# Kernel tuning notes

Hardware: AMD Instinct MI355X
Metric: run time of the kernel (lower is better)

## Reference

```python
import jax, jax.numpy as jnp
import numpy as np

LN2 = 0.6931471805599453
PI = 3.14159265

def ssp(x):
    # shifted softplus: log(exp(x)+1) - log(2)
    return jax.nn.softplus(x) - LN2

def setup_inputs() -> dict:
    key = jax.random.key(0)
    ks = jax.random.split(key, 16)
    N, E, R, F = 50000, 800000, 300, 64
    edge_index = jax.random.randint(ks[0], (2, E), 0, N, dtype=jnp.int64)
    node_feature = jax.random.normal(ks[1], (N, F), dtype=jnp.float32)
    rbf_tensor = jax.random.uniform(ks[2], (E, R), dtype=jnp.float32)
    cutoff = jnp.float32(10.0)
    dist = jax.random.uniform(ks[3], (E, 1), dtype=jnp.float32) * cutoff
    s = lambda fan_in: 1.0 / np.sqrt(fan_in)
    fw1 = jax.random.uniform(ks[4], (R, F), jnp.float32, -s(R), s(R))
    fb1 = jax.random.uniform(ks[5], (F,), jnp.float32, -s(R), s(R))
    fw2 = jax.random.uniform(ks[6], (F, F), jnp.float32, -s(F), s(F))
    fb2 = jax.random.uniform(ks[7], (F,), jnp.float32, -s(F), s(F))
    l1w = jax.random.uniform(ks[8], (F, F), jnp.float32, -s(F), s(F))
    l1b = jax.random.uniform(ks[9], (F,), jnp.float32, -s(F), s(F))
    l2w = jax.random.uniform(ks[10], (F, F), jnp.float32, -s(F), s(F))
    l2b = jax.random.uniform(ks[11], (F,), jnp.float32, -s(F), s(F))
    l3w = jax.random.uniform(ks[12], (F, F), jnp.float32, -s(F), s(F))
    l3b = jax.random.uniform(ks[13], (F,), jnp.float32, -s(F), s(F))
    return {"edge_index": edge_index, "node_feature": node_feature,
            "rbf_tensor": rbf_tensor, "dist": dist, "cutoff": cutoff,
            "fw1": fw1, "fb1": fb1, "fw2": fw2, "fb2": fb2,
            "l1w": l1w, "l1b": l1b, "l2w": l2w, "l2b": l2b,
            "l3w": l3w, "l3b": l3b}

def reference(edge_index, node_feature, rbf_tensor, dist, cutoff,
              fw1, fb1, fw2, fb2, l1w, l1b, l2w, l2b, l3w, l3b):
    N = node_feature.shape[0]
    x0 = node_feature  # residual
    h = node_feature @ l1w + l1b  # linear1: [N, F]
    # filter generator: two linear + shifted softplus layers on edge RBFs
    w = ssp(rbf_tensor @ fw1 + fb1)  # [E, F]
    w = ssp(w @ fw2 + fb2)           # [E, F]
    # cosine cutoff modulation ([E,1] broadcasts over F)
    w = w * (1.0 + jnp.cos(PI * dist / cutoff))
    # cfconv with flow='target_to_source': gather x_j from edge_index[1],
    # scatter-add into edge_index[0]
    msg = h[edge_index[1]] * w  # [E, F]
    agg = jax.ops.segment_sum(msg, edge_index[0], num_segments=N)  # [N, F]
    out = agg @ l2w + l2b
    out = ssp(out)
    out = out @ l3w + l3b
    return out + x0
```

## Files before the change

### kernel.cpp

```cpp
#include <hip/hip_runtime.h>
#include <hip/hip_bf16.h>
#include <math.h>

#define NNODES 50000
#define NEDGES 800000
#define RDIM   300
#define KPAD   320
#define LDA    328
#define LDW    72

typedef __attribute__((ext_vector_type(8))) short short8;
typedef __attribute__((ext_vector_type(4))) float floatx4;

__device__ __forceinline__ float ssp(float x) {
    return fmaxf(x, 0.0f) + log1pf(expf(-fabsf(x))) - 0.69314718056f;
}

__device__ __forceinline__ unsigned short f2bf(float f) {
    unsigned int u = __float_as_uint(f);
    unsigned int r = (u + 0x7FFFu + ((u >> 16) & 1u)) >> 16;
    return (unsigned short)r;
}

__global__ void prep_weights(const float* __restrict__ fw1, const float* __restrict__ fw2,
                             unsigned short* __restrict__ fw1t, unsigned short* __restrict__ fw2t) {
    int t = threadIdx.x + blockIdx.x * blockDim.x;
    int stride = blockDim.x * gridDim.x;
    for (int idx = t; idx < 64 * KPAD; idx += stride) {
        int n = idx / KPAD, k = idx - n * KPAD;
        float v = (k < RDIM) ? fw1[k * 64 + n] : 0.0f;
        fw1t[idx] = f2bf(v);
    }
    for (int idx = t; idx < 64 * 64; idx += stride) {
        int n = idx >> 6, k = idx & 63;
        fw2t[idx] = f2bf(fw2[k * 64 + n]);
    }
}

__global__ __launch_bounds__(256) void linear1_kernel(const float* __restrict__ x,
    const float* __restrict__ w, const float* __restrict__ b, float* __restrict__ h) {
    __shared__ float xs[64][65];
    __shared__ float ws[64][65];
    int t = threadIdx.x;
    int r0 = blockIdx.x * 64;
    for (int i = t; i < 4096; i += 256) ws[i >> 6][i & 63] = w[i];
    for (int i = t; i < 4096; i += 256) {
        int r = i >> 6;
        xs[r][i & 63] = (r0 + r < NNODES) ? x[(size_t)(r0 + r) * 64 + (i & 63)] : 0.0f;
    }
    __syncthreads();
    int c = t & 63;
    int rb = t >> 6;
    float bias = b[c];
    #pragma unroll 4
    for (int ri = 0; ri < 16; ri++) {
        int r = rb * 16 + ri;
        float acc = bias;
        #pragma unroll
        for (int k = 0; k < 64; k++) acc += xs[r][k] * ws[k][c];
        if (r0 + r < NNODES) h[(size_t)(r0 + r) * 64 + c] = acc;
    }
}

__global__ __launch_bounds__(256) void edge_kernel(
    const int* __restrict__ ei,
    const float* __restrict__ rbf,
    const float* __restrict__ dist,
    const float* __restrict__ cutoffp,
    const unsigned short* __restrict__ fw1t,
    const float* __restrict__ fb1,
    const unsigned short* __restrict__ fw2t,
    const float* __restrict__ fb2,
    const float* __restrict__ h,
    float* __restrict__ agg)
{
    __shared__ __align__(16) unsigned short rbf_s[64 * LDA];
    __shared__ __align__(16) unsigned short w1_s[64 * LDW];
    __shared__ float cut_s[64];
    __shared__ int src_s[64], dst_s[64];

    const int t = threadIdx.x;
    const int e0 = blockIdx.x * 64;
    const int lane = t & 63;
    const int wv = t >> 6;

    if (t < 64) {
        int e = e0 + t;
        dst_s[t] = ei[e];
        src_s[t] = ei[NEDGES + e];
        float co = *cutoffp;
        cut_s[t] = 1.0f + cosf(3.14159265f * dist[e] / co);
    }

    const int n = (wv << 4) + (lane & 15);
    const int kb = (lane >> 4) << 3;
    short8 b1[10];
    #pragma unroll
    for (int ks = 0; ks < 10; ks++)
        b1[ks] = *(const short8*)&fw1t[n * KPAD + ks * 32 + kb];
    short8 b2[2];
    #pragma unroll
    for (int ks = 0; ks < 2; ks++)
        b2[ks] = *(const short8*)&fw2t[n * 64 + ks * 32 + kb];
    const float fb1n = fb1[n];
    const float fb2n = fb2[n];

    {
        const float4* rp = (const float4*)(rbf + (size_t)e0 * RDIM);
        #pragma unroll
        for (int i = 0; i < 19; i++) {
            int idx4 = t + 256 * i;
            if (idx4 < 4800) {
                float4 v = rp[idx4];
                int row = idx4 / 75;
                int col4 = idx4 - row * 75;
                unsigned long long packed =
                    (unsigned long long)f2bf(v.x)
                  | ((unsigned long long)f2bf(v.y) << 16)
                  | ((unsigned long long)f2bf(v.z) << 32)
                  | ((unsigned long long)f2bf(v.w) << 48);
                *(unsigned long long*)&rbf_s[row * LDA + col4 * 4] = packed;
            }
        }
        if (t < 64) {
            #pragma unroll
            for (int c4 = 75; c4 < 80; c4++)
                *(unsigned long long*)&rbf_s[t * LDA + c4 * 4] = 0ULL;
        }
    }
    __syncthreads();

    const floatx4 zero4 = {0.0f, 0.0f, 0.0f, 0.0f};
    floatx4 acc[4] = {zero4, zero4, zero4, zero4};
    const int arow = lane & 15;
    #pragma unroll
    for (int ks = 0; ks < 10; ks++) {
        #pragma unroll
        for (int mt = 0; mt < 4; mt++) {
            short8 a = *(const short8*)&rbf_s[(mt * 16 + arow) * LDA + ks * 32 + kb];
            acc[mt] = __builtin_amdgcn_mfma_f32_16x16x32_bf16(a, b1[ks], acc[mt], 0, 0, 0);
        }
    }

    #pragma unroll
    for (int mt = 0; mt < 4; mt++) {
        #pragma unroll
        for (int r = 0; r < 4; r++) {
            int edge = mt * 16 + ((lane >> 4) << 2) + r;
            float v = ssp(acc[mt][r] + fb1n);
            w1_s[edge * LDW + n] = f2bf(v);
        }
    }
    __syncthreads();

    floatx4 acc2[4] = {zero4, zero4, zero4, zero4};
    #pragma unroll
    for (int ks = 0; ks < 2; ks++) {
        #pragma unroll
        for (int mt = 0; mt < 4; mt++) {
            short8 a = *(const short8*)&w1_s[(mt * 16 + arow) * LDW + ks * 32 + kb];
            acc2[mt] = __builtin_amdgcn_mfma_f32_16x16x32_bf16(a, b2[ks], acc2[mt], 0, 0, 0);
        }
    }

    #pragma unroll
    for (int mt = 0; mt < 4; mt++) {
        #pragma unroll
        for (int r = 0; r < 4; r++) {
            int el = mt * 16 + ((lane >> 4) << 2) + r;
            float w2v = ssp(acc2[mt][r] + fb2n) * cut_s[el];
            float msg = w2v * h[(size_t)src_s[el] * 64 + n];
            atomicAdd(&agg[(size_t)dst_s[el] * 64 + n], msg);
        }
    }
}

__global__ __launch_bounds__(256) void output_kernel(float* __restrict__ out,
    const float* __restrict__ x0,
    const float* __restrict__ l2w, const float* __restrict__ l2b,
    const float* __restrict__ l3w, const float* __restrict__ l3b) {
    __shared__ float as[64][65];
    __shared__ float w2s[64][65];
    __shared__ float w3s[64][65];
    __shared__ float ts[64][65];
    int t = threadIdx.x;
    int r0 = blockIdx.x * 64;
    for (int i = t; i < 4096; i += 256) w2s[i >> 6][i & 63] = l2w[i];
    for (int i = t; i < 4096; i += 256) w3s[i >> 6][i & 63] = l3w[i];
    for (int i = t; i < 4096; i += 256) {
        int r = i >> 6;
        as[r][i & 63] = (r0 + r < NNODES) ? out[(size_t)(r0 + r) * 64 + (i & 63)] : 0.0f;
    }
    __syncthreads();
    int c = t & 63;
    int rb = t >> 6;
    float b2 = l2b[c];
    #pragma unroll 4
    for (int ri = 0; ri < 16; ri++) {
        int r = rb * 16 + ri;
        float acc = b2;
        #pragma unroll
        for (int k = 0; k < 64; k++) acc += as[r][k] * w2s[k][c];
        ts[r][c] = ssp(acc);
    }
    __syncthreads();
    float b3 = l3b[c];
    #pragma unroll 4
    for (int ri = 0; ri < 16; ri++) {
        int r = rb * 16 + ri;
        float acc = b3;
        #pragma unroll
        for (int k = 0; k < 64; k++) acc += ts[r][k] * w3s[k][c];
        if (r0 + r < NNODES)
            out[(size_t)(r0 + r) * 64 + c] = acc + x0[(size_t)(r0 + r) * 64 + c];
    }
}

extern "C" void kernel_launch(void* const* d_in, const int* in_sizes, int n_in,
                              void* d_out, int out_size, void* d_ws, size_t ws_size,
                              hipStream_t stream) {
    const int* ei              = (const int*)d_in[0];
    const float* node_feature  = (const float*)d_in[1];
    const float* rbf           = (const float*)d_in[2];
    const float* dist          = (const float*)d_in[3];
    const float* cutoff        = (const float*)d_in[4];
    const float* fw1           = (const float*)d_in[5];
    const float* fb1           = (const float*)d_in[6];
    const float* fw2           = (const float*)d_in[7];
    const float* fb2           = (const float*)d_in[8];
    const float* l1w           = (const float*)d_in[9];
    const float* l1b           = (const float*)d_in[10];
    const float* l2w           = (const float*)d_in[11];
    const float* l2b           = (const float*)d_in[12];
    const float* l3w           = (const float*)d_in[13];
    const float* l3b           = (const float*)d_in[14];

    unsigned short* fw1t = (unsigned short*)d_ws;
    unsigned short* fw2t = (unsigned short*)((char*)d_ws + 40960);
    float* h = (float*)((char*)d_ws + 49152);
    float* agg = (float*)d_out;

    hipMemsetAsync(d_out, 0, (size_t)out_size * sizeof(float), stream);
    prep_weights<<<64, 256, 0, stream>>>(fw1, fw2, fw1t, fw2t);
    linear1_kernel<<<(NNODES + 63) / 64, 256, 0, stream>>>(node_feature, l1w, l1b, h);
    edge_kernel<<<NEDGES / 64, 256, 0, stream>>>(ei, rbf, dist, cutoff, fw1t, fb1, fw2t, fb2, h, agg);
    output_kernel<<<(NNODES + 63) / 64, 256, 0, stream>>>(agg, node_feature, l2w, l2b, l3w, l3b);
}
```

Baseline: 1.599 ms.

## Sort edges by destination and pre-reduce messages before atomic scatter

Builds a destination-sorted edge permutation via histogram, single-block scan and atomic scatter, then processes edges in sorted order. Messages are staged in shared memory and each wave reduces runs of equal destinations before issuing one atomic per run. This targets the cost of per-element global atomics, at the price of extra preprocessing kernels, a serial one-block scan, and gathered rather than contiguous rbf row reads.

```diff
diff --git a/kernel.cpp b/kernel.cpp
--- a/kernel.cpp
+++ b/kernel.cpp
@@ -8,6 +8,7 @@
 #define KPAD   320
 #define LDA    328
 #define LDW    72
+#define MSG_LD 66
 
 typedef __attribute__((ext_vector_type(8))) short short8;
 typedef __attribute__((ext_vector_type(4))) float floatx4;
@@ -62,8 +63,51 @@
     }
 }
 
+__global__ __launch_bounds__(256) void hist_kernel(const int* __restrict__ ei,
+                                                   int* __restrict__ deg) {
+    int e = threadIdx.x + blockIdx.x * 256;
+    if (e < NEDGES) atomicAdd(&deg[ei[e]], 1);
+}
+
+__global__ __launch_bounds__(1024) void scan_kernel(const int* __restrict__ deg,
+                                                    int* __restrict__ cursor) {
+    __shared__ int buf[1024];
+    __shared__ int base_s;
+    int t = threadIdx.x;
+    if (t == 0) base_s = 0;
+    __syncthreads();
+    for (int tile = 0; tile < NNODES; tile += 1024) {
+        int idx = tile + t;
+        int v = (idx < NNODES) ? deg[idx] : 0;
+        buf[t] = v;
+        __syncthreads();
+        for (int off = 1; off < 1024; off <<= 1) {
+            int self = buf[t];
+            int x = (t >= off) ? buf[t - off] : 0;
+            __syncthreads();
+            buf[t] = self + x;
+            __syncthreads();
+        }
+        if (idx < NNODES) cursor[idx] = base_s + buf[t] - v;
+        __syncthreads();
+        if (t == 0) base_s += buf[1023];
+        __syncthreads();
+    }
+}
+
+__global__ __launch_bounds__(256) void scatter_kernel(const int* __restrict__ ei,
+                                                      int* __restrict__ cursor,
+                                                      int* __restrict__ perm) {
+    int e = threadIdx.x + blockIdx.x * 256;
+    if (e < NEDGES) {
+        int slot = atomicAdd(&cursor[ei[e]], 1);
+        perm[slot] = e;
+    }
+}
+
 __global__ __launch_bounds__(256) void edge_kernel(
     const int* __restrict__ ei,
+    const int* __restrict__ perm,
     const float* __restrict__ rbf,
     const float* __restrict__ dist,
     const float* __restrict__ cutoffp,
@@ -77,7 +121,9 @@
     __shared__ __align__(16) unsigned short rbf_s[64 * LDA];
     __shared__ __align__(16) unsigned short w1_s[64 * LDW];
     __shared__ float cut_s[64];
-    __shared__ int src_s[64], dst_s[64];
+    __shared__ int src_s[64], dst_s[64], ep_s[64];
+
+    float (*msg_s)[MSG_LD] = (float (*)[MSG_LD])rbf_s;
 
     const int t = threadIdx.x;
     const int e0 = blockIdx.x * 64;
@@ -85,7 +131,8 @@
     const int wv = t >> 6;
 
     if (t < 64) {
-        int e = e0 + t;
+        int e = perm[e0 + t];
+        ep_s[t] = e;
         dst_s[t] = ei[e];
         src_s[t] = ei[NEDGES + e];
         float co = *cutoffp;
@@ -105,15 +152,17 @@
     const float fb1n = fb1[n];
     const float fb2n = fb2[n];
 
+    __syncthreads();
+
     {
-        const float4* rp = (const float4*)(rbf + (size_t)e0 * RDIM);
         #pragma unroll
         for (int i = 0; i < 19; i++) {
             int idx4 = t + 256 * i;
             if (idx4 < 4800) {
-                float4 v = rp[idx4];
                 int row = idx4 / 75;
                 int col4 = idx4 - row * 75;
+                const float4* rowp = (const float4*)(rbf + (size_t)ep_s[row] * RDIM);
+                float4 v = rowp[col4];
                 unsigned long long packed =
                     (unsigned long long)f2bf(v.x)
                   | ((unsigned long long)f2bf(v.y) << 16)
@@ -169,9 +218,27 @@
         for (int r = 0; r < 4; r++) {
             int el = mt * 16 + ((lane >> 4) << 2) + r;
             float w2v = ssp(acc2[mt][r] + fb2n) * cut_s[el];
-            float msg = w2v * h[(size_t)src_s[el] * 64 + n];
-            atomicAdd(&agg[(size_t)dst_s[el] * 64 + n], msg);
-        }
+            msg_s[el][n] = w2v * h[(size_t)src_s[el] * 64 + n];
+        }
+    }
+    __syncthreads();
+
+    {
+        const int c = lane;
+        const int r0 = wv * 16;
+        int cur = dst_s[r0];
+        float acc3 = 0.0f;
+        #pragma unroll
+        for (int r = r0; r < r0 + 16; ++r) {
+            int d = dst_s[r];
+            if (d != cur) {
+                atomicAdd(&agg[(size_t)cur * 64 + c], acc3);
+                acc3 = 0.0f;
+                cur = d;
+            }
+            acc3 += msg_s[r][c];
+        }
+        atomicAdd(&agg[(size_t)cur * 64 + c], acc3);
     }
 }
 
@@ -237,12 +304,20 @@
 
     unsigned short* fw1t = (unsigned short*)d_ws;
     unsigned short* fw2t = (unsigned short*)((char*)d_ws + 40960);
-    float* h = (float*)((char*)d_ws + 49152);
+    float* h    = (float*)((char*)d_ws + 49152);
+    int*   deg  = (int*)((char*)d_ws + 12849152);
+    int*   curs = (int*)((char*)d_ws + 13049152);
+    int*   perm = (int*)((char*)d_ws + 13249152);
     float* agg = (float*)d_out;
 
     hipMemsetAsync(d_out, 0, (size_t)out_size * sizeof(float), stream);
+    hipMemsetAsync(deg, 0, (size_t)NNODES * sizeof(int), stream);
     prep_weights<<<64, 256, 0, stream>>>(fw1, fw2, fw1t, fw2t);
     linear1_kernel<<<(NNODES + 63) / 64, 256, 0, stream>>>(node_feature, l1w, l1b, h);
-    edge_kernel<<<NEDGES / 64, 256, 0, stream>>>(ei, rbf, dist, cutoff, fw1t, fb1, fw2t, fb2, h, agg);
+    hist_kernel<<<NEDGES / 256, 256, 0, stream>>>(ei, deg);
+    scan_kernel<<<1, 1024, 0, stream>>>(deg, curs);
+    scatter_kernel<<<NEDGES / 256, 256, 0, stream>>>(ei, curs, perm);
+    edge_kernel<<<NEDGES / 64, 256, 0, stream>>>(ei, perm, rbf, dist, cutoff,
+                                                 fw1t, fb1, fw2t, fb2, h, agg);
     output_kernel<<<(NNODES + 63) / 64, 256, 0, stream>>>(agg, node_feature, l2w, l2b, l3w, l3b);
 }
```

Measured after the change: 1.771 ms. 10.7% more time.
